# Kernel tuning notes

Measured on AMD Instinct MI355X. Metric: run time of the kernel, lower is better.

Reference implementation:

```python
import jax, jax.numpy as jnp
import numpy as np

D_MODEL = 2048
NUM_HEADS = 32
NUM_GROUPS = 8
HEAD_DIM = D_MODEL // NUM_HEADS  # 64
HPG = NUM_HEADS // NUM_GROUPS    # heads per group = 4
B, S = 2, 2048


def setup_inputs() -> dict:
    key = jax.random.key(0)
    ks = jax.random.split(key, 11)
    sd = 1.0 / np.sqrt(D_MODEL)
    kv_dim = HEAD_DIM * NUM_GROUPS
    return {
        "q": jax.random.normal(ks[0], (B, S, D_MODEL), jnp.float32),
        "k": jax.random.normal(ks[1], (B, S, D_MODEL), jnp.float32),
        "v": jax.random.normal(ks[2], (B, S, D_MODEL), jnp.float32),
        "Wq": jax.random.normal(ks[3], (D_MODEL, D_MODEL), jnp.float32) * sd,
        "bq": jnp.zeros((D_MODEL,), jnp.float32),
        "Wk": jax.random.normal(ks[4], (D_MODEL, kv_dim), jnp.float32) * sd,
        "bk": jnp.zeros((kv_dim,), jnp.float32),
        "Wv": jax.random.normal(ks[5], (D_MODEL, kv_dim), jnp.float32) * sd,
        "bv": jnp.zeros((kv_dim,), jnp.float32),
        "Wo": jax.random.normal(ks[6], (D_MODEL, D_MODEL), jnp.float32) * sd,
        "bo": jnp.zeros((D_MODEL,), jnp.float32),
    }


def reference(q, k, v, Wq, bq, Wk, bk, Wv, bv, Wo, bo):
    b, qlen, _ = q.shape
    kvlen = k.shape[1]
    # projections
    qh = (q @ Wq + bq).reshape(b, qlen, NUM_GROUPS, HPG, HEAD_DIM)   # [b,s,g,h,d]
    kh = (k @ Wk + bk).reshape(b, kvlen, NUM_GROUPS, HEAD_DIM)        # [b,t,g,d]
    vh = (v @ Wv + bv).reshape(b, kvlen, NUM_GROUPS, HEAD_DIM)        # [b,t,g,d]
    scale = 1.0 / np.sqrt(HEAD_DIM).astype(np.float32)
    # grouped attention: each group's heads share the same K/V
    scores = jnp.einsum('bsghd,btgd->bghst', qh, kh) * scale          # [b,g,h,s,t]
    attn = jax.nn.softmax(scores, axis=-1)                            # dropout = identity (eval)
    out = jnp.einsum('bghst,btgd->bsghd', attn, vh)                   # [b,s,g,h,d]
    out = out.reshape(b, qlen, D_MODEL)
    return out @ Wo + bo
```

## Files before the change

kernel.cpp:

```cpp
#include <hip/hip_runtime.h>

typedef unsigned short u16;
typedef unsigned int u32;
typedef __attribute__((ext_vector_type(8))) short bf16x8;
typedef __attribute__((ext_vector_type(4))) float f32x4;
typedef __attribute__((ext_vector_type(16))) float f32x16;

#define DM 2048
#define SQ_SCALE (0.125f * 1.44269504089f)

__device__ __forceinline__ u16 f2bf(float f) {
  union { float f; u32 u; } v; v.f = f;
  u32 r = v.u + 0x7fffu + ((v.u >> 16) & 1u);
  return (u16)(r >> 16);
}
__device__ __forceinline__ u32 pkrn(float lo, float hi) {
  union { float f; u32 u; } a, b; a.f = lo; b.f = hi;
  return ((a.u + 0x8000u) >> 16) | ((b.u + 0x8000u) & 0xffff0000u);
}
__device__ __forceinline__ void gload16(const u16* g, u16* l) {
  __builtin_amdgcn_global_load_lds((const __attribute__((address_space(1))) void*)g,
                                   (__attribute__((address_space(3))) void*)l, 16, 0, 0);
}

__global__ __launch_bounds__(256) void cast3(const float* __restrict__ a0,
                                             const float* __restrict__ a1,
                                             const float* __restrict__ a2,
                                             u16* __restrict__ o0,
                                             u16* __restrict__ o1,
                                             u16* __restrict__ o2) {
  const float* in; u16* out;
  if (blockIdx.z == 0) { in = a0; out = o0; }
  else if (blockIdx.z == 1) { in = a1; out = o1; }
  else { in = a2; out = o2; }
  size_t i = ((size_t)blockIdx.x * 256 + threadIdx.x) * 8;
  float4 f0 = *(const float4*)(in + i);
  float4 f1 = *(const float4*)(in + i + 4);
  uint4 w = {pkrn(f0.x, f0.y), pkrn(f0.z, f0.w), pkrn(f1.x, f1.y), pkrn(f1.z, f1.w)};
  *(uint4*)(out + i) = w;
}

__global__ __launch_bounds__(256) void transpose_cast(const float* __restrict__ in,
                                                      u16* __restrict__ out,
                                                      int K, int N) {
  __shared__ u16 s[64][72];
  int n0 = blockIdx.x * 64, k0 = blockIdx.y * 64;
  int t = threadIdx.x;
  int r = t >> 2;
  int cc = (t & 3) * 16;
  const float* ip = in + (size_t)(k0 + r) * N + n0 + cc;
  u16 tmp[16];
#pragma unroll
  for (int i = 0; i < 16; i += 4) {
    float4 v = *(const float4*)(ip + i);
    tmp[i] = f2bf(v.x); tmp[i + 1] = f2bf(v.y);
    tmp[i + 2] = f2bf(v.z); tmp[i + 3] = f2bf(v.w);
  }
  *(uint4*)&s[r][cc] = *(uint4*)tmp;
  *(uint4*)&s[r][cc + 8] = *(uint4*)(tmp + 8);
  __syncthreads();
#pragma unroll
  for (int i = 0; i < 16; i++) tmp[i] = s[cc + i][r];
  u16* op = out + (size_t)(n0 + r) * K + k0 + cc;
  *(uint4*)op = *(uint4*)tmp;
  *(uint4*)(op + 8) = *(uint4*)(tmp + 8);
}

__global__ __launch_bounds__(256) void transpose_v(const u16* __restrict__ kvb,
                                                   u16* __restrict__ vtb) {
  __shared__ u16 s[64][72];
  int bg = blockIdx.y;
  int t0 = blockIdx.x * 64;
  int t = threadIdx.x;
  int r = t >> 2;
  int cc = (t & 3) * 16;
  const u16* ip = kvb + ((size_t)(bg >> 3) * 2048 + t0 + r) * 1024 + 512 + (bg & 7) * 64 + cc;
  *(uint4*)&s[r][cc] = *(const uint4*)ip;
  *(uint4*)&s[r][cc + 8] = *(const uint4*)(ip + 8);
  __syncthreads();
  u16 tmp[16];
#pragma unroll
  for (int i = 0; i < 16; i++) tmp[i] = s[cc + i][r];
  u16* op = vtb + (size_t)bg * 64 * 2048 + (size_t)r * 2048 + t0 + cc;
  *(uint4*)op = *(uint4*)tmp;
  *(uint4*)(op + 8) = *(uint4*)(tmp + 8);
}

__global__ __launch_bounds__(256) void gemm_proj(const u16* __restrict__ qb,
                                                 const u16* __restrict__ kb,
                                                 const u16* __restrict__ vb,
                                                 const u16* __restrict__ Bt,
                                                 const float* __restrict__ bqp,
                                                 const float* __restrict__ bkp,
                                                 const float* __restrict__ bvp,
                                                 u16* __restrict__ qhb,
                                                 u16* __restrict__ kvb) {
  __shared__ u16 As[128 * 32];
  __shared__ u16 Bs[128 * 32];
  int n0 = blockIdx.x * 128, m0 = blockIdx.y * 128;
  const u16* A; const float* bias; u16* C; int cw, bofs; float esc;
  if (n0 < 2048)      { A = qb; bias = bqp; C = qhb; cw = 2048; bofs = 0;    esc = SQ_SCALE; }
  else if (n0 < 2560) { A = kb; bias = bkp; C = kvb; cw = 1024; bofs = 2048; esc = 1.0f; }
  else                { A = vb; bias = bvp; C = kvb; cw = 1024; bofs = 2560; esc = 1.0f; }
  int ccol0 = (n0 < 2048) ? n0 : (n0 - 2048);

  int tid = threadIdx.x, wave = tid >> 6, lane = tid & 63;
  int lq = lane & 15, quad = lane >> 4;
  int wm = (wave & 1) * 64, wn = (wave >> 1) * 64;

  f32x4 zero = {0.f, 0.f, 0.f, 0.f};
  f32x4 acc[4][4];
#pragma unroll
  for (int i = 0; i < 4; i++)
#pragma unroll
    for (int j = 0; j < 4; j++) acc[i][j] = zero;

  const u16* gA = A + (size_t)(m0 + wave * 16 + (lane >> 2)) * 2048 + (lane & 3) * 8;
  const u16* gB = Bt + (size_t)(n0 + wave * 16 + (lane >> 2)) * 2048 + (lane & 3) * 8;
  u16* lA0 = &As[(wave * 16) * 32];
  u16* lA1 = &As[(64 + wave * 16) * 32];
  u16* lB0 = &Bs[(wave * 16) * 32];
  u16* lB1 = &Bs[(64 + wave * 16) * 32];

  for (int k0 = 0; k0 < 2048; k0 += 32) {
    __syncthreads();
    gload16(gA + k0, lA0);
    gload16(gA + (size_t)64 * 2048 + k0, lA1);
    gload16(gB + k0, lB0);
    gload16(gB + (size_t)64 * 2048 + k0, lB1);
    __syncthreads();
    bf16x8 af[4], bf[4];
#pragma unroll
    for (int i = 0; i < 4; i++) af[i] = *(const bf16x8*)&As[(wm + i * 16 + lq) * 32 + quad * 8];
#pragma unroll
    for (int j = 0; j < 4; j++) bf[j] = *(const bf16x8*)&Bs[(wn + j * 16 + lq) * 32 + quad * 8];
#pragma unroll
    for (int i = 0; i < 4; i++)
#pragma unroll
      for (int j = 0; j < 4; j++)
        acc[i][j] = __builtin_amdgcn_mfma_f32_16x16x32_bf16(af[i], bf[j], acc[i][j], 0, 0, 0);
  }
#pragma unroll
  for (int j = 0; j < 4; j++) {
    int nglob = n0 + wn + j * 16 + lq;
    float bv = bias[nglob - bofs];
    int col = ccol0 + wn + j * 16 + lq;
#pragma unroll
    for (int i = 0; i < 4; i++) {
#pragma unroll
      for (int rg = 0; rg < 4; rg++) {
        int row = m0 + wm + i * 16 + quad * 4 + rg;
        C[(size_t)row * cw + col] = f2bf((acc[i][j][rg] + bv) * esc);
      }
    }
  }
}

__global__ __launch_bounds__(256) void gemm_o(const u16* __restrict__ A,
                                              const u16* __restrict__ Bt,
                                              const float* __restrict__ bias,
                                              float* __restrict__ C) {
  __shared__ u16 As[128 * 32];
  __shared__ u16 Bs[128 * 32];
  int n0 = blockIdx.x * 128, m0 = blockIdx.y * 128;
  int tid = threadIdx.x, wave = tid >> 6, lane = tid & 63;
  int lq = lane & 15, quad = lane >> 4;
  int wm = (wave & 1) * 64, wn = (wave >> 1) * 64;

  f32x4 zero = {0.f, 0.f, 0.f, 0.f};
  f32x4 acc[4][4];
#pragma unroll
  for (int i = 0; i < 4; i++)
#pragma unroll
    for (int j = 0; j < 4; j++) acc[i][j] = zero;

  const u16* gA = A + (size_t)(m0 + wave * 16 + (lane >> 2)) * 2048 + (lane & 3) * 8;
  const u16* gB = Bt + (size_t)(n0 + wave * 16 + (lane >> 2)) * 2048 + (lane & 3) * 8;
  u16* lA0 = &As[(wave * 16) * 32];
  u16* lA1 = &As[(64 + wave * 16) * 32];
  u16* lB0 = &Bs[(wave * 16) * 32];
  u16* lB1 = &Bs[(64 + wave * 16) * 32];

  for (int k0 = 0; k0 < 2048; k0 += 32) {
    __syncthreads();
    gload16(gA + k0, lA0);
    gload16(gA + (size_t)64 * 2048 + k0, lA1);
    gload16(gB + k0, lB0);
    gload16(gB + (size_t)64 * 2048 + k0, lB1);
    __syncthreads();
    bf16x8 af[4], bf[4];
#pragma unroll
    for (int i = 0; i < 4; i++) af[i] = *(const bf16x8*)&As[(wm + i * 16 + lq) * 32 + quad * 8];
#pragma unroll
    for (int j = 0; j < 4; j++) bf[j] = *(const bf16x8*)&Bs[(wn + j * 16 + lq) * 32 + quad * 8];
#pragma unroll
    for (int i = 0; i < 4; i++)
#pragma unroll
      for (int j = 0; j < 4; j++)
        acc[i][j] = __builtin_amdgcn_mfma_f32_16x16x32_bf16(af[i], bf[j], acc[i][j], 0, 0, 0);
  }
#pragma unroll
  for (int j = 0; j < 4; j++) {
    int col = n0 + wn + j * 16 + lq;
    float bv = bias[col];
#pragma unroll
    for (int i = 0; i < 4; i++) {
#pragma unroll
      for (int rg = 0; rg < 4; rg++) {
        int row = m0 + wm + i * 16 + quad * 4 + rg;
        C[(size_t)row * 2048 + col] = acc[i][j][rg] + bv;
      }
    }
  }
}

__global__ __launch_bounds__(256) void attn2(const u16* __restrict__ qh,
                                             const u16* __restrict__ kvb,
                                             const u16* __restrict__ vtb,
                                             u16* __restrict__ out) {
  __shared__ u16 Ks[32][72];
  __shared__ u16 Vs[64][40];
  __shared__ float Ls[4][2][32];
  int head = blockIdx.y;
  int b = head >> 5, g = (head >> 2) & 7, h = head & 3;
  int tid = threadIdx.x, wave = tid >> 6, lane = tid & 63;
  int lh = lane & 31, hi = lane >> 5;
  const int qoff = (g * 4 + h) * 64;
  const int koff = g * 64;
  int sBase = blockIdx.x * 256 + wave * 64;

  bf16x8 qf[2][4];
#pragma unroll
  for (int sb = 0; sb < 2; sb++)
#pragma unroll
    for (int st = 0; st < 4; st++)
      qf[sb][st] = *(const bf16x8*)(qh + (size_t)(b * 2048 + sBase + sb * 32 + lh) * DM +
                                    qoff + st * 16 + hi * 8);

  f32x16 o_acc[2][2];
#pragma unroll
  for (int sb = 0; sb < 2; sb++)
#pragma unroll
    for (int db = 0; db < 2; db++)
#pragma unroll
      for (int r = 0; r < 16; r++) o_acc[sb][db][r] = 0.f;
  float l_acc[2] = {0.f, 0.f};

  int sr = tid >> 3, sc = (tid & 7) * 8;
  int vd = tid >> 2, vc = (tid & 3) * 8;
  const u16* kbase = kvb + (size_t)b * 2048 * 1024 + koff;
  const u16* vbase = vtb + (size_t)(head >> 2) * 64 * 2048 + (size_t)vd * 2048;

  uint4 kreg = *(const uint4*)(kbase + (size_t)sr * 1024 + sc);
  uint4 vreg = *(const uint4*)(vbase + vc);

  for (int t0 = 0; t0 < 2048; t0 += 32) {
    __syncthreads();
    *(uint4*)&Ks[sr][sc] = kreg;
    *(uint4*)&Vs[vd][vc] = vreg;
    __syncthreads();
    int tn = (t0 + 32 < 2048) ? t0 + 32 : 0;
    kreg = *(const uint4*)(kbase + (size_t)(tn + sr) * 1024 + sc);
    vreg = *(const uint4*)(vbase + tn + vc);

    bf16x8 kf[4], vf[2][2];
#pragma unroll
    for (int st = 0; st < 4; st++) kf[st] = *(const bf16x8*)&Ks[lh][st * 16 + hi * 8];
#pragma unroll
    for (int T = 0; T < 2; T++)
#pragma unroll
      for (int db = 0; db < 2; db++)
        vf[T][db] = *(const bf16x8*)&Vs[db * 32 + lh][T * 16 + hi * 8];

#pragma unroll
    for (int sb = 0; sb < 2; sb++) {
      f32x16 st_acc;
#pragma unroll
      for (int r = 0; r < 16; r++) st_acc[r] = 0.f;
#pragma unroll
      for (int st = 0; st < 4; st++)
        st_acc = __builtin_amdgcn_mfma_f32_32x32x16_bf16(kf[st], qf[sb][st], st_acc, 0, 0, 0);
      float pr[16];
#pragma unroll
      for (int r = 0; r < 16; r++) pr[r] = __builtin_amdgcn_exp2f(st_acc[r]);
      float s0 = ((pr[0] + pr[1]) + (pr[2] + pr[3])) + ((pr[4] + pr[5]) + (pr[6] + pr[7]));
      float s1 = ((pr[8] + pr[9]) + (pr[10] + pr[11])) + ((pr[12] + pr[13]) + (pr[14] + pr[15]));
      l_acc[sb] += s0 + s1;
      u32 pk[8];
#pragma unroll
      for (int a = 0; a < 4; a++) {
        pk[2 * a] = pkrn(pr[4 * a], pr[4 * a + 1]);
        pk[2 * a + 1] = pkrn(pr[4 * a + 2], pr[4 * a + 3]);
      }
#pragma unroll
      for (int T = 0; T < 2; T++) {
        u32 E0 = hi ? pk[4 * T] : pk[4 * T + 2];
        u32 E1 = hi ? pk[4 * T + 1] : pk[4 * T + 3];
        u32 X0 = __shfl_xor(E0, 32);
        u32 X1 = __shfl_xor(E1, 32);
        union { u32 u[4]; bf16x8 v; } af;
        af.u[0] = hi ? X0 : pk[4 * T];
        af.u[1] = hi ? X1 : pk[4 * T + 1];
        af.u[2] = hi ? pk[4 * T + 2] : X0;
        af.u[3] = hi ? pk[4 * T + 3] : X1;
#pragma unroll
        for (int db = 0; db < 2; db++)
          o_acc[sb][db] = __builtin_amdgcn_mfma_f32_32x32x16_bf16(af.v, vf[T][db], o_acc[sb][db], 0, 0, 0);
      }
    }
  }

#pragma unroll
  for (int sb = 0; sb < 2; sb++) {
    float lt = l_acc[sb] + __shfl_xor(l_acc[sb], 32);
    Ls[wave][sb][lh] = 1.0f / lt;
  }
  __builtin_amdgcn_wave_barrier();
#pragma unroll
  for (int sb = 0; sb < 2; sb++) {
    f32x4 inv[4];
#pragma unroll
    for (int a = 0; a < 4; a++) inv[a] = *(const f32x4*)&Ls[wave][sb][8 * a + 4 * hi];
#pragma unroll
    for (int db = 0; db < 2; db++) {
#pragma unroll
      for (int r = 0; r < 16; r++) {
        int srow = (r & 3) + 8 * (r >> 2) + 4 * hi;
        size_t o = (size_t)(b * 2048 + sBase + sb * 32 + srow) * DM + qoff + db * 32 + lh;
        out[o] = f2bf(o_acc[sb][db][r] * inv[r >> 2][r & 3]);
      }
    }
  }
}

extern "C" void kernel_launch(void* const* d_in, const int* in_sizes, int n_in,
                              void* d_out, int out_size, void* d_ws, size_t ws_size,
                              hipStream_t stream) {
  const float* q  = (const float*)d_in[0];
  const float* k  = (const float*)d_in[1];
  const float* v  = (const float*)d_in[2];
  const float* Wq = (const float*)d_in[3];
  const float* bq = (const float*)d_in[4];
  const float* Wk = (const float*)d_in[5];
  const float* bk = (const float*)d_in[6];
  const float* Wv = (const float*)d_in[7];
  const float* bv = (const float*)d_in[8];
  const float* Wo = (const float*)d_in[9];
  const float* bo = (const float*)d_in[10];

  u16* p = (u16*)d_ws;
  u16* WqkvT = p; p += (size_t)3072 * 2048;
  u16* WoT   = p; p += (size_t)2048 * 2048;
  u16* qb    = p; p += (size_t)4096 * 2048;
  u16* kb    = p; p += (size_t)4096 * 2048;
  u16* vb    = p; p += (size_t)4096 * 2048;
  u16* qhb   = p; p += (size_t)4096 * 2048;
  u16* kvb   = p; p += (size_t)4096 * 1024;
  u16* vtb   = p; p += (size_t)16 * 64 * 2048;
  u16* att   = qb;

  cast3<<<dim3(4096, 1, 3), 256, 0, stream>>>(q, k, v, qb, kb, vb);

  transpose_cast<<<dim3(32, 32), 256, 0, stream>>>(Wq, WqkvT, 2048, 2048);
  transpose_cast<<<dim3(8, 32), 256, 0, stream>>>(Wk, WqkvT + (size_t)2048 * 2048, 2048, 512);
  transpose_cast<<<dim3(8, 32), 256, 0, stream>>>(Wv, WqkvT + (size_t)2560 * 2048, 2048, 512);
  transpose_cast<<<dim3(32, 32), 256, 0, stream>>>(Wo, WoT, 2048, 2048);

  gemm_proj<<<dim3(24, 32), 256, 0, stream>>>(qb, kb, vb, WqkvT, bq, bk, bv, qhb, kvb);

  transpose_v<<<dim3(32, 16), 256, 0, stream>>>(kvb, vtb);

  attn2<<<dim3(8, 64), 256, 0, stream>>>(qhb, kvb, vtb, att);

  gemm_o<<<dim3(16, 32), 256, 0, stream>>>(att, WoT, bo, (float*)d_out);
}
```

Baseline: 405.0 us.

## Halve per-wave query rows, compute softmax denominator via MFMA with ones

The attention kernel now gives each wave 32 query rows instead of 64 and launches twice as many blocks, which raises occupancy and parallelism but reloads K/V tiles into shared memory twice as often. The row-sum of probabilities is computed by an extra MFMA against a ones vector, replacing scalar adds, cross-lane shuffles and the shared-memory reciprocal exchange. Packing to bf16 uses a truncating byte-permute instead of round-to-nearest, which cuts ALU work at some cost in precision.

```diff
diff --git a/kernel.cpp b/kernel.cpp
--- a/kernel.cpp
+++ b/kernel.cpp
@@ -17,6 +17,10 @@
 __device__ __forceinline__ u32 pkrn(float lo, float hi) {
   union { float f; u32 u; } a, b; a.f = lo; b.f = hi;
   return ((a.u + 0x8000u) >> 16) | ((b.u + 0x8000u) & 0xffff0000u);
+}
+__device__ __forceinline__ u32 pktr(float lo, float hi) {
+  union { float f; u32 u; } a, b; a.f = lo; b.f = hi;
+  return __builtin_amdgcn_perm(b.u, a.u, 0x07060302u);
 }
 __device__ __forceinline__ void gload16(const u16* g, u16* l) {
   __builtin_amdgcn_global_load_lds((const __attribute__((address_space(1))) void*)g,
@@ -214,37 +218,32 @@
   }
 }
 
-__global__ __launch_bounds__(256) void attn2(const u16* __restrict__ qh,
+__global__ __launch_bounds__(256) void attn4(const u16* __restrict__ qh,
                                              const u16* __restrict__ kvb,
                                              const u16* __restrict__ vtb,
                                              u16* __restrict__ out) {
   __shared__ u16 Ks[32][72];
   __shared__ u16 Vs[64][40];
-  __shared__ float Ls[4][2][32];
   int head = blockIdx.y;
+  int schunk = blockIdx.x;
   int b = head >> 5, g = (head >> 2) & 7, h = head & 3;
   int tid = threadIdx.x, wave = tid >> 6, lane = tid & 63;
   int lh = lane & 31, hi = lane >> 5;
   const int qoff = (g * 4 + h) * 64;
   const int koff = g * 64;
-  int sBase = blockIdx.x * 256 + wave * 64;
-
-  bf16x8 qf[2][4];
-#pragma unroll
-  for (int sb = 0; sb < 2; sb++)
-#pragma unroll
-    for (int st = 0; st < 4; st++)
-      qf[sb][st] = *(const bf16x8*)(qh + (size_t)(b * 2048 + sBase + sb * 32 + lh) * DM +
-                                    qoff + st * 16 + hi * 8);
-
-  f32x16 o_acc[2][2];
-#pragma unroll
-  for (int sb = 0; sb < 2; sb++)
-#pragma unroll
-    for (int db = 0; db < 2; db++)
-#pragma unroll
-      for (int r = 0; r < 16; r++) o_acc[sb][db][r] = 0.f;
-  float l_acc[2] = {0.f, 0.f};
+  int sBase = schunk * 128 + wave * 32;
+
+  bf16x8 qf[4];
+#pragma unroll
+  for (int st = 0; st < 4; st++)
+    qf[st] = *(const bf16x8*)(qh + (size_t)(b * 2048 + sBase + lh) * DM + qoff + st * 16 + hi * 8);
+
+  f32x16 o0, o1, lac;
+#pragma unroll
+  for (int r = 0; r < 16; r++) { o0[r] = 0.f; o1[r] = 0.f; lac[r] = 0.f; }
+
+  const bf16x8 ones = {(short)0x3F80, (short)0x3F80, (short)0x3F80, (short)0x3F80,
+                       (short)0x3F80, (short)0x3F80, (short)0x3F80, (short)0x3F80};
 
   int sr = tid >> 3, sc = (tid & 7) * 8;
   int vd = tid >> 2, vc = (tid & 3) * 8;
@@ -272,64 +271,46 @@
       for (int db = 0; db < 2; db++)
         vf[T][db] = *(const bf16x8*)&Vs[db * 32 + lh][T * 16 + hi * 8];
 
-#pragma unroll
-    for (int sb = 0; sb < 2; sb++) {
-      f32x16 st_acc;
-#pragma unroll
-      for (int r = 0; r < 16; r++) st_acc[r] = 0.f;
-#pragma unroll
-      for (int st = 0; st < 4; st++)
-        st_acc = __builtin_amdgcn_mfma_f32_32x32x16_bf16(kf[st], qf[sb][st], st_acc, 0, 0, 0);
-      float pr[16];
-#pragma unroll
-      for (int r = 0; r < 16; r++) pr[r] = __builtin_amdgcn_exp2f(st_acc[r]);
-      float s0 = ((pr[0] + pr[1]) + (pr[2] + pr[3])) + ((pr[4] + pr[5]) + (pr[6] + pr[7]));
-      float s1 = ((pr[8] + pr[9]) + (pr[10] + pr[11])) + ((pr[12] + pr[13]) + (pr[14] + pr[15]));
-      l_acc[sb] += s0 + s1;
-      u32 pk[8];
-#pragma unroll
-      for (int a = 0; a < 4; a++) {
-        pk[2 * a] = pkrn(pr[4 * a], pr[4 * a + 1]);
-        pk[2 * a + 1] = pkrn(pr[4 * a + 2], pr[4 * a + 3]);
-      }
-#pragma unroll
-      for (int T = 0; T < 2; T++) {
-        u32 E0 = hi ? pk[4 * T] : pk[4 * T + 2];
-        u32 E1 = hi ? pk[4 * T + 1] : pk[4 * T + 3];
-        u32 X0 = __shfl_xor(E0, 32);
-        u32 X1 = __shfl_xor(E1, 32);
-        union { u32 u[4]; bf16x8 v; } af;
-        af.u[0] = hi ? X0 : pk[4 * T];
-        af.u[1] = hi ? X1 : pk[4 * T + 1];
-        af.u[2] = hi ? pk[4 * T + 2] : X0;
-        af.u[3] = hi ? pk[4 * T + 3] : X1;
-#pragma unroll
-        for (int db = 0; db < 2; db++)
-          o_acc[sb][db] = __builtin_amdgcn_mfma_f32_32x32x16_bf16(af.v, vf[T][db], o_acc[sb][db], 0, 0, 0);
-      }
+    f32x16 st_acc;
+#pragma unroll
+    for (int r = 0; r < 16; r++) st_acc[r] = 0.f;
+#pragma unroll
+    for (int st = 0; st < 4; st++)
+      st_acc = __builtin_amdgcn_mfma_f32_32x32x16_bf16(kf[st], qf[st], st_acc, 0, 0, 0);
+
+    float pr[16];
+#pragma unroll
+    for (int r = 0; r < 16; r++) pr[r] = __builtin_amdgcn_exp2f(st_acc[r]);
+    u32 pk[8];
+#pragma unroll
+    for (int a = 0; a < 4; a++) {
+      pk[2 * a] = pktr(pr[4 * a], pr[4 * a + 1]);
+      pk[2 * a + 1] = pktr(pr[4 * a + 2], pr[4 * a + 3]);
     }
-  }
-
-#pragma unroll
-  for (int sb = 0; sb < 2; sb++) {
-    float lt = l_acc[sb] + __shfl_xor(l_acc[sb], 32);
-    Ls[wave][sb][lh] = 1.0f / lt;
-  }
-  __builtin_amdgcn_wave_barrier();
-#pragma unroll
-  for (int sb = 0; sb < 2; sb++) {
-    f32x4 inv[4];
-#pragma unroll
-    for (int a = 0; a < 4; a++) inv[a] = *(const f32x4*)&Ls[wave][sb][8 * a + 4 * hi];
-#pragma unroll
-    for (int db = 0; db < 2; db++) {
-#pragma unroll
-      for (int r = 0; r < 16; r++) {
-        int srow = (r & 3) + 8 * (r >> 2) + 4 * hi;
-        size_t o = (size_t)(b * 2048 + sBase + sb * 32 + srow) * DM + qoff + db * 32 + lh;
-        out[o] = f2bf(o_acc[sb][db][r] * inv[r >> 2][r & 3]);
-      }
+#pragma unroll
+    for (int T = 0; T < 2; T++) {
+      u32 E0 = hi ? pk[4 * T] : pk[4 * T + 2];
+      u32 E1 = hi ? pk[4 * T + 1] : pk[4 * T + 3];
+      u32 X0 = __shfl_xor(E0, 32);
+      u32 X1 = __shfl_xor(E1, 32);
+      union { u32 u[4]; bf16x8 v; } af;
+      af.u[0] = hi ? X0 : pk[4 * T];
+      af.u[1] = hi ? X1 : pk[4 * T + 1];
+      af.u[2] = hi ? pk[4 * T + 2] : X0;
+      af.u[3] = hi ? pk[4 * T + 3] : X1;
+      lac = __builtin_amdgcn_mfma_f32_32x32x16_bf16(af.v, ones, lac, 0, 0, 0);
+      o0 = __builtin_amdgcn_mfma_f32_32x32x16_bf16(af.v, vf[T][0], o0, 0, 0, 0);
+      o1 = __builtin_amdgcn_mfma_f32_32x32x16_bf16(af.v, vf[T][1], o1, 0, 0, 0);
     }
+  }
+
+#pragma unroll
+  for (int r = 0; r < 16; r++) {
+    float inv = 1.0f / lac[r];
+    int srow = (r & 3) + 8 * (r >> 2) + 4 * hi;
+    size_t base = (size_t)(b * 2048 + sBase + srow) * DM + qoff + lh;
+    out[base] = f2bf(o0[r] * inv);
+    out[base + 32] = f2bf(o1[r] * inv);
   }
 }
 
@@ -370,7 +351,7 @@
 
   transpose_v<<<dim3(32, 16), 256, 0, stream>>>(kvb, vtb);
 
-  attn2<<<dim3(8, 64), 256, 0, stream>>>(qhb, kvb, vtb, att);
+  attn4<<<dim3(16, 64), 256, 0, stream>>>(qhb, kvb, vtb, att);
 
   gemm_o<<<dim3(16, 32), 256, 0, stream>>>(att, WoT, bo, (float*)d_out);
 }
```

Result: slower. 417.1 us (+3.0%).
